# Optimization experiments

Measured on AMD Instinct MI355X. Metric: run time of the kernel, lower is better.

## Reference

```python
import jax, jax.numpy as jnp
import numpy as np

N_NODES = 50000
N_EDGES = 800000
F_IN = 24
H = 128
N_GRAPHS = 100
BN_EPS = 1e-5


def setup_inputs() -> dict:
    key = jax.random.key(0)
    ks = jax.random.split(key, 12)
    x = jax.random.normal(ks[0], (N_NODES, F_IN), dtype=jnp.float32)
    edge_index = jax.random.randint(ks[1], (2, N_EDGES), 0, N_NODES, dtype=jnp.int32)
    batch = (jnp.arange(N_NODES, dtype=jnp.int32) // (N_NODES // N_GRAPHS)).astype(jnp.int32)

    def lin(k, fan_in, fan_out):
        bound = 1.0 / np.sqrt(fan_in)
        kw, kb = jax.random.split(k)
        W = jax.random.uniform(kw, (fan_in, fan_out), jnp.float32, -bound, bound)
        b = jax.random.uniform(kb, (fan_out,), jnp.float32, -bound, bound)
        return W, b

    W1, b1 = lin(ks[2], 2 * F_IN, H)
    W2, b2 = lin(ks[3], 2 * H, H)
    W3, b3 = lin(ks[4], 2 * H, H)
    Wl, bl = lin(ks[5], H, 1)
    g1 = jnp.ones((H,), jnp.float32); be1 = jnp.zeros((H,), jnp.float32)
    g2 = jnp.ones((H,), jnp.float32); be2 = jnp.zeros((H,), jnp.float32)
    g3 = jnp.ones((H,), jnp.float32); be3 = jnp.zeros((H,), jnp.float32)
    return {"x": x, "edge_index": edge_index, "batch": batch,
            "W1": W1, "b1": b1, "W2": W2, "b2": b2, "W3": W3, "b3": b3,
            "g1": g1, "be1": be1, "g2": g2, "be2": be2, "g3": g3, "be3": be3,
            "Wl": Wl, "bl": bl}


def edge_conv(x, src, dst, W, b):
    # PyG EdgeConv: message = mlp([x_i, x_j - x_i]) for edge j->i, aggr=max at i
    x_i = x[dst]                                    # [E, F]
    e = jnp.concatenate([x_i, x[src] - x_i], axis=-1)  # [E, 2F]
    m = jax.nn.relu(e @ W + b)                      # [E, H]
    out = jax.ops.segment_max(m, dst, num_segments=N_NODES)
    return jnp.where(jnp.isfinite(out), out, 0.0)   # isolated nodes -> 0


def batch_norm(h, g, b):
    # training-mode BN over node dim (biased variance), dropout treated as identity
    mu = h.mean(axis=0)
    var = ((h - mu) ** 2).mean(axis=0)
    return g * (h - mu) * jax.lax.rsqrt(var + BN_EPS) + b


def reference(x, edge_index, batch, W1, b1, W2, b2, W3, b3,
              g1, be1, g2, be2, g3, be3, Wl, bl):
    src, dst = edge_index[0], edge_index[1]
    h = edge_conv(x, src, dst, W1, b1)
    h = jax.nn.relu(batch_norm(h, g1, be1))
    h = edge_conv(h, src, dst, W2, b2)
    h = jax.nn.relu(batch_norm(h, g2, be2))
    h = edge_conv(h, src, dst, W3, b3)
    h = batch_norm(h, g3, be3)
    # global_mean_pool
    sums = jax.ops.segment_sum(h, batch, num_segments=N_GRAPHS)           # [G, H]
    counts = jax.ops.segment_sum(jnp.ones((h.shape[0],), h.dtype), batch,
                                 num_segments=N_GRAPHS)
    pooled = sums / jnp.maximum(counts, 1.0)[:, None]
    return jax.nn.relu(pooled @ Wl + bl)                                  # [G, 1]
```

## Files before the change

kernel.cpp:

```cpp
#include <hip/hip_runtime.h>

#define N_NODES 50000
#define N_EDGES 800000
#define F_IN 24
#define HDIM 128
#define N_GRAPHS 100
#define BN_EPS 1e-5f
#define NBLK 196
#define ROWS_PER_GRAPH (N_NODES / N_GRAPHS)
#define MM_GRID 782
#define HIST_BLKS ((N_EDGES + 255) / 256)
#define PREP_BLKS (F_IN + 2 * HDIM)
#define SSTR 32
#define SUMS_PER_LAYER (256 * SSTR)
#define STATS_BLKS 196

typedef _Float16 h2 __attribute__((ext_vector_type(2)));
typedef _Float16 h4 __attribute__((ext_vector_type(4)));
typedef _Float16 f16x8 __attribute__((ext_vector_type(8)));
typedef float f32x4 __attribute__((ext_vector_type(4)));

template <int K, int KC>
__global__ __launch_bounds__(256) void k_mm1(const float* __restrict__ X,
                                             const float* __restrict__ Wcat,
                                             const float* __restrict__ bias,
                                             float* __restrict__ A, _Float16* __restrict__ C) {
    __shared__ float Xs[KC * 68];
    __shared__ float Ws[KC * 128];
    int tid = threadIdx.x;
    int row0 = blockIdx.x * 64;
    const bool isA = (blockIdx.y == 0);
    const int colbase = isA ? 0 : 128;
    int cg = tid & 31;
    int rg = tid >> 5;

    float acc[8][4];
#pragma unroll
    for (int ri = 0; ri < 8; ++ri)
#pragma unroll
        for (int ci = 0; ci < 4; ++ci)
            acc[ri][ci] = isA ? bias[cg * 4 + ci] : 0.f;

    for (int k0 = 0; k0 < K; k0 += KC) {
        __syncthreads();
        {
            const int C4 = KC / 4;
            for (int i = tid; i < 64 * C4; i += 256) {
                int c4 = i % C4, r = i / C4;
                int row = row0 + r;
                float4 v = make_float4(0.f, 0.f, 0.f, 0.f);
                if (row < N_NODES) v = *(const float4*)&X[row * K + k0 + c4 * 4];
                Xs[(c4 * 4 + 0) * 68 + r] = v.x;
                Xs[(c4 * 4 + 1) * 68 + r] = v.y;
                Xs[(c4 * 4 + 2) * 68 + r] = v.z;
                Xs[(c4 * 4 + 3) * 68 + r] = v.w;
            }
        }
        for (int i = tid; i < KC * 32; i += 256) {
            int c4 = i & 31, kr = i >> 5;
            *(float4*)&Ws[kr * 128 + c4 * 4] =
                *(const float4*)&Wcat[(k0 + kr) * 256 + colbase + c4 * 4];
        }
        __syncthreads();
#pragma unroll
        for (int kk = 0; kk < KC; ++kk) {
            float4 t0 = *(const float4*)&Xs[kk * 68 + rg * 8];
            float4 t1 = *(const float4*)&Xs[kk * 68 + rg * 8 + 4];
            float4 w = *(const float4*)&Ws[kk * 128 + cg * 4];
            float t[8] = {t0.x, t0.y, t0.z, t0.w, t1.x, t1.y, t1.z, t1.w};
            float wv[4] = {w.x, w.y, w.z, w.w};
#pragma unroll
            for (int ri = 0; ri < 8; ++ri)
#pragma unroll
                for (int ci = 0; ci < 4; ++ci)
                    acc[ri][ci] += t[ri] * wv[ci];
        }
    }

#pragma unroll
    for (int ri = 0; ri < 8; ++ri) {
        int row = row0 + rg * 8 + ri;
        if (row < N_NODES) {
            if (isA) {
                *(float4*)&A[row * HDIM + cg * 4] =
                    make_float4(acc[ri][0], acc[ri][1], acc[ri][2], acc[ri][3]);
            } else {
                union { h2 h[2]; uint2 u; } pk;
                pk.h[0] = h2{(_Float16)acc[ri][0], (_Float16)acc[ri][1]};
                pk.h[1] = h2{(_Float16)acc[ri][2], (_Float16)acc[ri][3]};
                *(uint2*)&C[row * HDIM + cg * 4] = pk.u;
            }
        }
    }
}

__global__ __launch_bounds__(256) void k_mmf(const _Float16* __restrict__ X,
                                             const _Float16* __restrict__ Wf,
                                             const float* __restrict__ bias,
                                             const float* __restrict__ sums,
                                             const float* __restrict__ g,
                                             const float* __restrict__ be,
                                             float* __restrict__ A, _Float16* __restrict__ C) {
    __shared__ _Float16 Xh[16 * 520];
    __shared__ _Float16 Wh[128 * 128];
    __shared__ float scs[128], shs[128];
    int tid = threadIdx.x;
    int lane = tid & 63, wv = tid >> 6;
    int row0 = blockIdx.x * 64;
    const bool isA = (blockIdx.y == 0);
    const _Float16* Wsrc = Wf + (isA ? 0 : 16384);

    if (tid < 128) {
        float S  = sums[tid * SSTR];
        float S2 = sums[(128 + tid) * SSTR];
        float mean = S / (float)N_NODES;
        float var = fmaxf(S2 / (float)N_NODES - mean * mean, 0.f);
        float scv = g[tid] / sqrtf(var + BN_EPS);
        scs[tid] = scv;
        shs[tid] = be[tid] - mean * scv;
    }
    {
        const uint4* s = (const uint4*)Wsrc;
        uint4* d = (uint4*)Wh;
        for (int i = tid; i < 2048; i += 256) d[i] = s[i];
    }
    __syncthreads();
    for (int i = tid; i < 64 * 32; i += 256) {
        int k4 = i & 31, rl = i >> 5;
        int row = row0 + rl;
        float4 v = make_float4(0.f, 0.f, 0.f, 0.f);
        if (row < N_NODES) {
            h4 xv = *(const h4*)&X[row * HDIM + k4 * 4];
            v = make_float4((float)xv.x, (float)xv.y, (float)xv.z, (float)xv.w);
        }
        int c = k4 * 4;
        v.x = fmaxf(v.x * scs[c + 0] + shs[c + 0], 0.f);
        v.y = fmaxf(v.y * scs[c + 1] + shs[c + 1], 0.f);
        v.z = fmaxf(v.z * scs[c + 2] + shs[c + 2], 0.f);
        v.w = fmaxf(v.w * scs[c + 3] + shs[c + 3], 0.f);
        int rt = rl >> 4, m = rl & 15, kc = k4 >> 3, q = (k4 >> 1) & 3, jh = k4 & 1;
        _Float16* d = Xh + (rt * 4 + kc) * 520 + (q * 16 + m) * 8 + jh * 4;
        d[0] = (_Float16)v.x; d[1] = (_Float16)v.y;
        d[2] = (_Float16)v.z; d[3] = (_Float16)v.w;
    }
    __syncthreads();

    int n = lane & 15, q = lane >> 4;
    f32x4 acc[8];
#pragma unroll
    for (int nt = 0; nt < 8; ++nt) {
        float b0 = isA ? bias[nt * 16 + n] : 0.f;
        acc[nt] = f32x4{b0, b0, b0, b0};
    }
#pragma unroll
    for (int kc = 0; kc < 4; ++kc) {
        f16x8 a = *(const f16x8*)(Xh + (wv * 4 + kc) * 520 + lane * 8);
#pragma unroll
        for (int nt = 0; nt < 8; ++nt) {
            f16x8 b = *(const f16x8*)(Wh + ((nt * 4 + kc) * 64 + lane) * 8);
            acc[nt] = __builtin_amdgcn_mfma_f32_16x16x32_f16(a, b, acc[nt], 0, 0, 0);
        }
    }
#pragma unroll
    for (int nt = 0; nt < 8; ++nt) {
#pragma unroll
        for (int r = 0; r < 4; ++r) {
            int row = row0 + wv * 16 + q * 4 + r;
            if (row < N_NODES) {
                int col = nt * 16 + n;
                if (isA) A[row * HDIM + col] = acc[nt][r];
                else     C[row * HDIM + col] = (_Float16)acc[nt][r];
            }
        }
    }
}

__global__ void k_pre(const float* __restrict__ W1, const float* __restrict__ W2,
                      const float* __restrict__ W3, float* __restrict__ Wcat1,
                      _Float16* __restrict__ Wf2, _Float16* __restrict__ Wf3,
                      const int* __restrict__ dst, unsigned* __restrict__ deg,
                      unsigned* __restrict__ rank) {
    int b = blockIdx.x;
    int j = threadIdx.x;
    if (b < F_IN) {
        float wb = W1[(b + F_IN) * HDIM + (j & 127)];
        float wt = W1[b * HDIM + (j & 127)];
        Wcat1[b * 256 + j] = (j < HDIM) ? (wt - wb) : wb;
    } else if (b < PREP_BLKS) {
        int idx = b - F_IN;
        int layer = idx >> 7;
        int k = idx & 127;
        const float* W = layer ? W3 : W2;
        _Float16* Wf   = layer ? Wf3 : Wf2;
        int col = j & 127;
        float wt = W[k * HDIM + col];
        float wb = W[(k + HDIM) * HDIM + col];
        float v = (j < 128) ? (wt - wb) : wb;
        int plane = j >> 7;
        int nt = col >> 4, n = col & 15, kc = k >> 5, q = (k >> 3) & 3, jj = k & 7;
        int f = ((nt * 4 + kc) * 4 + q) * 128 + n * 8 + jj;
        Wf[plane * 16384 + f] = (_Float16)v;
    } else {
        int e = (b - PREP_BLKS) * 256 + j;
        if (e < N_EDGES) rank[e] = atomicAdd(&deg[dst[e]], 1u);
    }
}

__global__ __launch_bounds__(256) void k_scanall(const unsigned* __restrict__ deg,
                                                 unsigned* __restrict__ bsum,
                                                 unsigned* __restrict__ off) {
    __shared__ unsigned s[256];
    int t = threadIdx.x;
    int b = blockIdx.x;
    int i = b * 256 + t;
    unsigned v = (i < N_NODES) ? deg[i] : 0u;
    s[t] = v;
    __syncthreads();
    for (int d = 1; d < 256; d <<= 1) {
        unsigned u = (t >= d) ? s[t - d] : 0u;
        __syncthreads();
        s[t] += u;
        __syncthreads();
    }
    unsigned locex = s[t] - v;
    if (t == 255) atomicExch(&bsum[b], s[255] + 1u);
    __syncthreads();
    unsigned bs = 0;
    if (t < NBLK) {
        unsigned x;
        do { x = atomicAdd(&bsum[t], 0u); } while (x == 0u);
        bs = x - 1u;
    }
    s[t] = (t < NBLK) ? bs : 0u;
    __syncthreads();
    for (int d = 1; d < 256; d <<= 1) {
        unsigned u = (t >= d) ? s[t - d] : 0u;
        __syncthreads();
        s[t] += u;
        __syncthreads();
    }
    unsigned bexcl = (b == 0) ? 0u : s[b - 1];
    if (i < N_NODES) off[i] = bexcl + locex;
}

__global__ void k_scatter(const int* __restrict__ src, const int* __restrict__ dst,
                          const unsigned* __restrict__ off, const unsigned* __restrict__ rank,
                          unsigned* __restrict__ ssrc) {
    int e = blockIdx.x * 256 + threadIdx.x;
    if (e < N_EDGES)
        ssrc[off[dst[e]] + rank[e]] = (unsigned)src[e];
}

__global__ __launch_bounds__(256) void k_agg(const float* __restrict__ A,
                                             const h2* __restrict__ Cc,
                                             const unsigned* __restrict__ off,
                                             const unsigned* __restrict__ deg,
                                             const unsigned* __restrict__ ssrc,
                                             h2* __restrict__ H) {
    __shared__ unsigned sl[4][64];
    int w = threadIdx.x >> 6;
    int lane = threadIdx.x & 63;
    int i = blockIdx.x * 4 + w;
    int d = (int)deg[i];
    unsigned o = off[i];
    union { unsigned short us[2]; h2 v; } ninf;
    ninf.us[0] = 0xFC00; ninf.us[1] = 0xFC00;
    h2 m2 = ninf.v;
    for (int base = 0; base < d; base += 64) {
        int cntc = min(64, d - base);
        if (lane < cntc) sl[w][lane] = ssrc[o + base + lane];
        int e = 0;
        for (; e + 8 <= cntc; e += 8) {
            unsigned s0 = sl[w][e + 0], s1 = sl[w][e + 1], s2 = sl[w][e + 2], s3 = sl[w][e + 3];
            unsigned s4 = sl[w][e + 4], s5 = sl[w][e + 5], s6 = sl[w][e + 6], s7 = sl[w][e + 7];
            h2 v0 = Cc[s0 * 64 + lane];
            h2 v1 = Cc[s1 * 64 + lane];
            h2 v2 = Cc[s2 * 64 + lane];
            h2 v3 = Cc[s3 * 64 + lane];
            h2 v4 = Cc[s4 * 64 + lane];
            h2 v5 = Cc[s5 * 64 + lane];
            h2 v6 = Cc[s6 * 64 + lane];
            h2 v7 = Cc[s7 * 64 + lane];
            h2 a0 = __builtin_elementwise_max(v0, v1);
            h2 a1 = __builtin_elementwise_max(v2, v3);
            h2 a2 = __builtin_elementwise_max(v4, v5);
            h2 a3 = __builtin_elementwise_max(v6, v7);
            h2 b0 = __builtin_elementwise_max(a0, a1);
            h2 b1 = __builtin_elementwise_max(a2, a3);
            m2 = __builtin_elementwise_max(m2, __builtin_elementwise_max(b0, b1));
        }
        if (e + 4 <= cntc) {
            unsigned s0 = sl[w][e + 0], s1 = sl[w][e + 1], s2 = sl[w][e + 2], s3 = sl[w][e + 3];
            h2 v0 = Cc[s0 * 64 + lane];
            h2 v1 = Cc[s1 * 64 + lane];
            h2 v2 = Cc[s2 * 64 + lane];
            h2 v3 = Cc[s3 * 64 + lane];
            h2 a0 = __builtin_elementwise_max(v0, v1);
            h2 a1 = __builtin_elementwise_max(v2, v3);
            m2 = __builtin_elementwise_max(m2, __builtin_elementwise_max(a0, a1));
            e += 4;
        }
        for (; e < cntc; ++e)
            m2 = __builtin_elementwise_max(m2, Cc[sl[w][e] * 64 + lane]);
    }
    float2 a = *(const float2*)&A[i * HDIM + lane * 2];
    float hx = (d > 0) ? fmaxf(a.x + (float)m2.x, 0.f) : 0.f;
    float hy = (d > 0) ? fmaxf(a.y + (float)m2.y, 0.f) : 0.f;
    H[i * 64 + lane] = h2{(_Float16)hx, (_Float16)hy};
}

__global__ __launch_bounds__(256) void k_stats(const _Float16* __restrict__ H,
                                               float* __restrict__ sums) {
    __shared__ float4 ls[256], ls2[256];
    int t = threadIdx.x;
    int c4 = t & 31, rg = t >> 5;
    int row0 = blockIdx.x * 256;
    float4 s = make_float4(0.f, 0.f, 0.f, 0.f);
    float4 s2 = make_float4(0.f, 0.f, 0.f, 0.f);
#pragma unroll 4
    for (int it = 0; it < 32; ++it) {
        int row = row0 + rg * 32 + it;
        if (row < N_NODES) {
            h4 hv = *(const h4*)&H[row * HDIM + c4 * 4];
            float4 v = make_float4((float)hv.x, (float)hv.y, (float)hv.z, (float)hv.w);
            s.x += v.x; s.y += v.y; s.z += v.z; s.w += v.w;
            s2.x += v.x * v.x; s2.y += v.y * v.y; s2.z += v.z * v.z; s2.w += v.w * v.w;
        }
    }
    ls[t] = s; ls2[t] = s2;
    __syncthreads();
    if (t < 32) {
        float4 a = ls[t], a2 = ls2[t];
#pragma unroll
        for (int j = 1; j < 8; ++j) {
            float4 b = ls[j * 32 + t], b2 = ls2[j * 32 + t];
            a.x += b.x; a.y += b.y; a.z += b.z; a.w += b.w;
            a2.x += b2.x; a2.y += b2.y; a2.z += b2.z; a2.w += b2.w;
        }
        int c = t * 4;
        atomicAdd(&sums[(c + 0) * SSTR], a.x);
        atomicAdd(&sums[(c + 1) * SSTR], a.y);
        atomicAdd(&sums[(c + 2) * SSTR], a.z);
        atomicAdd(&sums[(c + 3) * SSTR], a.w);
        atomicAdd(&sums[(128 + c + 0) * SSTR], a2.x);
        atomicAdd(&sums[(128 + c + 1) * SSTR], a2.y);
        atomicAdd(&sums[(128 + c + 2) * SSTR], a2.z);
        atomicAdd(&sums[(128 + c + 3) * SSTR], a2.w);
    }
}

__global__ __launch_bounds__(128) void k_poolsum(const _Float16* __restrict__ H,
                                                 float* __restrict__ Pg,
                                                 float* __restrict__ sums) {
    int g = blockIdx.x;
    int k = threadIdx.x;
    const _Float16* base = H + (size_t)g * ROWS_PER_GRAPH * HDIM;
    float s = 0.f, s2 = 0.f;
#pragma unroll 4
    for (int r = 0; r < ROWS_PER_GRAPH; ++r) {
        float v = (float)base[r * HDIM + k];
        s += v; s2 += v * v;
    }
    Pg[g * HDIM + k] = s;
    atomicAdd(&sums[k * SSTR], s);
    atomicAdd(&sums[(128 + k) * SSTR], s2);
}

__global__ __launch_bounds__(128) void k_out(const float* __restrict__ Pg,
                                             const float* __restrict__ sums,
                                             const float* __restrict__ g3,
                                             const float* __restrict__ be3,
                                             const float* __restrict__ Wl,
                                             const float* __restrict__ bl,
                                             float* __restrict__ out) {
    int g = blockIdx.x;
    int k = threadIdx.x;
    float S  = sums[k * SSTR];
    float S2 = sums[(128 + k) * SSTR];
    float mean = S / (float)N_NODES;
    float var = fmaxf(S2 / (float)N_NODES - mean * mean, 0.f);
    float scv = g3[k] / sqrtf(var + BN_EPS);
    float shv = be3[k] - mean * scv;
    float p = (scv * (Pg[g * HDIM + k] * (1.f / (float)ROWS_PER_GRAPH)) + shv) * Wl[k];
    __shared__ float red[2];
    for (int o = 32; o > 0; o >>= 1) p += __shfl_down(p, o);
    if ((k & 63) == 0) red[k >> 6] = p;
    __syncthreads();
    if (k == 0) out[g] = fmaxf(red[0] + red[1] + bl[0], 0.f);
}

extern "C" void kernel_launch(void* const* d_in, const int* in_sizes, int n_in,
                              void* d_out, int out_size, void* d_ws, size_t ws_size,
                              hipStream_t stream) {
    const float* x   = (const float*)d_in[0];
    const int* ei    = (const int*)d_in[1];
    const float* W1  = (const float*)d_in[3];
    const float* b1  = (const float*)d_in[4];
    const float* W2  = (const float*)d_in[5];
    const float* b2  = (const float*)d_in[6];
    const float* W3  = (const float*)d_in[7];
    const float* b3  = (const float*)d_in[8];
    const float* g1  = (const float*)d_in[9];
    const float* be1 = (const float*)d_in[10];
    const float* g2  = (const float*)d_in[11];
    const float* be2 = (const float*)d_in[12];
    const float* g3  = (const float*)d_in[13];
    const float* be3 = (const float*)d_in[14];
    const float* Wl  = (const float*)d_in[15];
    const float* bl  = (const float*)d_in[16];
    float* out = (float*)d_out;

    const int* srcp = ei;
    const int* dstp = ei + N_EDGES;

    char* ws = (char*)d_ws;
    size_t o = 0;
    auto alloc = [&](size_t bytes) -> void* {
        o = (o + 255) & ~(size_t)255;
        void* p = ws + o;
        o += bytes;
        return p;
    };
    float* A      = (float*)alloc((size_t)N_NODES * HDIM * 4);
    _Float16* C   = (_Float16*)alloc((size_t)N_NODES * HDIM * 2);
    _Float16* h   = (_Float16*)alloc((size_t)N_NODES * HDIM * 2);
    float* Wcat1  = (float*)alloc((size_t)F_IN * 256 * 4);
    _Float16* Wf2 = (_Float16*)alloc((size_t)2 * 16384 * 2);
    _Float16* Wf3 = (_Float16*)alloc((size_t)2 * 16384 * 2);
    unsigned* deg  = (unsigned*)alloc((size_t)N_NODES * 4);
    unsigned* bsum = (unsigned*)alloc((size_t)NBLK * 4);
    float* sums    = (float*)alloc((size_t)3 * SUMS_PER_LAYER * 4);
    unsigned* off  = (unsigned*)alloc((size_t)N_NODES * 4);
    unsigned* rank = (unsigned*)alloc((size_t)N_EDGES * 4);
    unsigned* ssrc = (unsigned*)alloc((size_t)N_EDGES * 4);
    float* Pg      = (float*)alloc((size_t)N_GRAPHS * HDIM * 4);
    (void)ws_size; (void)n_in; (void)in_sizes; (void)out_size;

    float* sums0 = sums;
    float* sums1 = sums + SUMS_PER_LAYER;
    float* sums2 = sums + 2 * SUMS_PER_LAYER;

    size_t zlen = (size_t)((char*)(sums + 3 * SUMS_PER_LAYER) - (char*)deg);
    (void)hipMemsetAsync(deg, 0, zlen, stream);

    k_pre<<<PREP_BLKS + HIST_BLKS, 256, 0, stream>>>(W1, W2, W3, Wcat1, Wf2, Wf3,
                                                     dstp, deg, rank);
    k_scanall<<<NBLK, 256, 0, stream>>>(deg, bsum, off);
    k_scatter<<<HIST_BLKS, 256, 0, stream>>>(srcp, dstp, off, rank, ssrc);

    const dim3 MMG(MM_GRID, 2);
    const int AGB = N_NODES / 4;

    k_mm1<F_IN, F_IN><<<MMG, 256, 0, stream>>>(x, Wcat1, b1, A, C);
    k_agg<<<AGB, 256, 0, stream>>>(A, (const h2*)C, off, deg, ssrc, (h2*)h);
    k_stats<<<STATS_BLKS, 256, 0, stream>>>(h, sums0);

    k_mmf<<<MMG, 256, 0, stream>>>(h, Wf2, b2, sums0, g1, be1, A, C);
    k_agg<<<AGB, 256, 0, stream>>>(A, (const h2*)C, off, deg, ssrc, (h2*)h);
    k_stats<<<STATS_BLKS, 256, 0, stream>>>(h, sums1);

    k_mmf<<<MMG, 256, 0, stream>>>(h, Wf3, b3, sums1, g2, be2, A, C);
    k_agg<<<AGB, 256, 0, stream>>>(A, (const h2*)C, off, deg, ssrc, (h2*)h);

    k_poolsum<<<N_GRAPHS, 128, 0, stream>>>(h, Pg, sums2);
    k_out<<<N_GRAPHS, 128, 0, stream>>>(Pg, sums2, g3, be3, Wl, bl, out);
}
```

Baseline: 400.4 us.

## Fuse BN statistics and mean-pool accumulation into aggregation kernel epilogue

Removes the separate k_stats and k_poolsum kernels and computes per-channel sum and sum-of-squares inside k_agg's epilogue. The partial sums are spread across 98 group slots per channel to cut atomic contention, and consumers (k_mmf, k_out) reduce those slots on load. The aim is to avoid re-reading h from memory and to save two kernel launches per layer. In exchange, stats now use fp32 values before fp16 rounding, each k_agg block adds a barrier plus atomics, and every mmf block re-reduces the partial slots.

```diff
diff --git a/kernel.cpp b/kernel.cpp
--- a/kernel.cpp
+++ b/kernel.cpp
@@ -11,9 +11,9 @@
 #define MM_GRID 782
 #define HIST_BLKS ((N_EDGES + 255) / 256)
 #define PREP_BLKS (F_IN + 2 * HDIM)
-#define SSTR 32
-#define SUMS_PER_LAYER (256 * SSTR)
-#define STATS_BLKS 196
+#define AGB (N_NODES / 4)
+#define NGRP 98
+#define SGRP 104
 
 typedef _Float16 h2 __attribute__((ext_vector_type(2)));
 typedef _Float16 h4 __attribute__((ext_vector_type(4)));
@@ -97,12 +97,13 @@
 __global__ __launch_bounds__(256) void k_mmf(const _Float16* __restrict__ X,
                                              const _Float16* __restrict__ Wf,
                                              const float* __restrict__ bias,
-                                             const float* __restrict__ sums,
+                                             const float* __restrict__ sumsP,
                                              const float* __restrict__ g,
                                              const float* __restrict__ be,
                                              float* __restrict__ A, _Float16* __restrict__ C) {
     __shared__ _Float16 Xh[16 * 520];
     __shared__ _Float16 Wh[128 * 128];
+    __shared__ float Srow[256];
     __shared__ float scs[128], shs[128];
     int tid = threadIdx.x;
     int lane = tid & 63, wv = tid >> 6;
@@ -110,19 +111,31 @@
     const bool isA = (blockIdx.y == 0);
     const _Float16* Wsrc = Wf + (isA ? 0 : 16384);
 
+    {
+        const float* rp = sumsP + tid * SGRP;
+        float s = 0.f;
+#pragma unroll
+        for (int j = 0; j < 24; ++j) {
+            float4 v = *(const float4*)&rp[j * 4];
+            s += v.x + v.y + v.z + v.w;
+        }
+        s += rp[96] + rp[97];
+        Srow[tid] = s;
+    }
+    {
+        const uint4* s = (const uint4*)Wsrc;
+        uint4* d = (uint4*)Wh;
+        for (int i = tid; i < 2048; i += 256) d[i] = s[i];
+    }
+    __syncthreads();
     if (tid < 128) {
-        float S  = sums[tid * SSTR];
-        float S2 = sums[(128 + tid) * SSTR];
+        float S  = Srow[tid];
+        float S2 = Srow[128 + tid];
         float mean = S / (float)N_NODES;
         float var = fmaxf(S2 / (float)N_NODES - mean * mean, 0.f);
         float scv = g[tid] / sqrtf(var + BN_EPS);
         scs[tid] = scv;
         shs[tid] = be[tid] - mean * scv;
-    }
-    {
-        const uint4* s = (const uint4*)Wsrc;
-        uint4* d = (uint4*)Wh;
-        for (int i = tid; i < 2048; i += 256) d[i] = s[i];
     }
     __syncthreads();
     for (int i = tid; i < 64 * 32; i += 256) {
@@ -251,13 +264,18 @@
         ssrc[off[dst[e]] + rank[e]] = (unsigned)src[e];
 }
 
+template <bool POOL>
 __global__ __launch_bounds__(256) void k_agg(const float* __restrict__ A,
                                              const h2* __restrict__ Cc,
                                              const unsigned* __restrict__ off,
                                              const unsigned* __restrict__ deg,
                                              const unsigned* __restrict__ ssrc,
-                                             h2* __restrict__ H) {
+                                             h2* __restrict__ H,
+                                             float* __restrict__ sumsP,
+                                             float* __restrict__ Pg) {
     __shared__ unsigned sl[4][64];
+    __shared__ float2 ps[4][64];
+    __shared__ float2 ps2[4][64];
     int w = threadIdx.x >> 6;
     int lane = threadIdx.x & 63;
     int i = blockIdx.x * 4 + w;
@@ -307,67 +325,33 @@
     float hx = (d > 0) ? fmaxf(a.x + (float)m2.x, 0.f) : 0.f;
     float hy = (d > 0) ? fmaxf(a.y + (float)m2.y, 0.f) : 0.f;
     H[i * 64 + lane] = h2{(_Float16)hx, (_Float16)hy};
-}
-
-__global__ __launch_bounds__(256) void k_stats(const _Float16* __restrict__ H,
-                                               float* __restrict__ sums) {
-    __shared__ float4 ls[256], ls2[256];
-    int t = threadIdx.x;
-    int c4 = t & 31, rg = t >> 5;
-    int row0 = blockIdx.x * 256;
-    float4 s = make_float4(0.f, 0.f, 0.f, 0.f);
-    float4 s2 = make_float4(0.f, 0.f, 0.f, 0.f);
-#pragma unroll 4
-    for (int it = 0; it < 32; ++it) {
-        int row = row0 + rg * 32 + it;
-        if (row < N_NODES) {
-            h4 hv = *(const h4*)&H[row * HDIM + c4 * 4];
-            float4 v = make_float4((float)hv.x, (float)hv.y, (float)hv.z, (float)hv.w);
-            s.x += v.x; s.y += v.y; s.z += v.z; s.w += v.w;
-            s2.x += v.x * v.x; s2.y += v.y * v.y; s2.z += v.z * v.z; s2.w += v.w * v.w;
-        }
-    }
-    ls[t] = s; ls2[t] = s2;
-    __syncthreads();
-    if (t < 32) {
-        float4 a = ls[t], a2 = ls2[t];
-#pragma unroll
-        for (int j = 1; j < 8; ++j) {
-            float4 b = ls[j * 32 + t], b2 = ls2[j * 32 + t];
-            a.x += b.x; a.y += b.y; a.z += b.z; a.w += b.w;
-            a2.x += b2.x; a2.y += b2.y; a2.z += b2.z; a2.w += b2.w;
-        }
-        int c = t * 4;
-        atomicAdd(&sums[(c + 0) * SSTR], a.x);
-        atomicAdd(&sums[(c + 1) * SSTR], a.y);
-        atomicAdd(&sums[(c + 2) * SSTR], a.z);
-        atomicAdd(&sums[(c + 3) * SSTR], a.w);
-        atomicAdd(&sums[(128 + c + 0) * SSTR], a2.x);
-        atomicAdd(&sums[(128 + c + 1) * SSTR], a2.y);
-        atomicAdd(&sums[(128 + c + 2) * SSTR], a2.z);
-        atomicAdd(&sums[(128 + c + 3) * SSTR], a2.w);
-    }
-}
-
-__global__ __launch_bounds__(128) void k_poolsum(const _Float16* __restrict__ H,
-                                                 float* __restrict__ Pg,
-                                                 float* __restrict__ sums) {
-    int g = blockIdx.x;
-    int k = threadIdx.x;
-    const _Float16* base = H + (size_t)g * ROWS_PER_GRAPH * HDIM;
-    float s = 0.f, s2 = 0.f;
-#pragma unroll 4
-    for (int r = 0; r < ROWS_PER_GRAPH; ++r) {
-        float v = (float)base[r * HDIM + k];
-        s += v; s2 += v * v;
-    }
-    Pg[g * HDIM + k] = s;
-    atomicAdd(&sums[k * SSTR], s);
-    atomicAdd(&sums[(128 + k) * SSTR], s2);
+
+    ps[w][lane]  = float2{hx, hy};
+    ps2[w][lane] = float2{hx * hx, hy * hy};
+    __syncthreads();
+    if (w == 0) {
+        float sx = 0.f, sy = 0.f, qx = 0.f, qy = 0.f;
+#pragma unroll
+        for (int j = 0; j < 4; ++j) {
+            float2 p = ps[j][lane], p2 = ps2[j][lane];
+            sx += p.x; sy += p.y; qx += p2.x; qy += p2.y;
+        }
+        int grp = blockIdx.x >> 7;
+        int c0 = lane * 2;
+        atomicAdd(&sumsP[(c0 + 0) * SGRP + grp], sx);
+        atomicAdd(&sumsP[(c0 + 1) * SGRP + grp], sy);
+        atomicAdd(&sumsP[(128 + c0) * SGRP + grp], qx);
+        atomicAdd(&sumsP[(129 + c0) * SGRP + grp], qy);
+        if (POOL) {
+            int graph = (blockIdx.x * 4) / ROWS_PER_GRAPH;
+            atomicAdd(&Pg[graph * HDIM + c0], sx);
+            atomicAdd(&Pg[graph * HDIM + c0 + 1], sy);
+        }
+    }
 }
 
 __global__ __launch_bounds__(128) void k_out(const float* __restrict__ Pg,
-                                             const float* __restrict__ sums,
+                                             const float* __restrict__ sumsP,
                                              const float* __restrict__ g3,
                                              const float* __restrict__ be3,
                                              const float* __restrict__ Wl,
@@ -375,8 +359,18 @@
                                              float* __restrict__ out) {
     int g = blockIdx.x;
     int k = threadIdx.x;
-    float S  = sums[k * SSTR];
-    float S2 = sums[(128 + k) * SSTR];
+    const float* r1 = sumsP + k * SGRP;
+    const float* r2 = sumsP + (128 + k) * SGRP;
+    float S = 0.f, S2 = 0.f;
+#pragma unroll
+    for (int j = 0; j < 24; ++j) {
+        float4 a = *(const float4*)&r1[j * 4];
+        float4 b = *(const float4*)&r2[j * 4];
+        S  += a.x + a.y + a.z + a.w;
+        S2 += b.x + b.y + b.z + b.w;
+    }
+    S  += r1[96] + r1[97];
+    S2 += r2[96] + r2[97];
     float mean = S / (float)N_NODES;
     float var = fmaxf(S2 / (float)N_NODES - mean * mean, 0.f);
     float scv = g3[k] / sqrtf(var + BN_EPS);
@@ -429,18 +423,16 @@
     _Float16* Wf3 = (_Float16*)alloc((size_t)2 * 16384 * 2);
     unsigned* deg  = (unsigned*)alloc((size_t)N_NODES * 4);
     unsigned* bsum = (unsigned*)alloc((size_t)NBLK * 4);
-    float* sums    = (float*)alloc((size_t)3 * SUMS_PER_LAYER * 4);
+    float* sums0P  = (float*)alloc((size_t)256 * SGRP * 4);
+    float* sums1P  = (float*)alloc((size_t)256 * SGRP * 4);
+    float* sums2P  = (float*)alloc((size_t)256 * SGRP * 4);
+    float* Pg      = (float*)alloc((size_t)N_GRAPHS * HDIM * 4);
     unsigned* off  = (unsigned*)alloc((size_t)N_NODES * 4);
     unsigned* rank = (unsigned*)alloc((size_t)N_EDGES * 4);
     unsigned* ssrc = (unsigned*)alloc((size_t)N_EDGES * 4);
-    float* Pg      = (float*)alloc((size_t)N_GRAPHS * HDIM * 4);
     (void)ws_size; (void)n_in; (void)in_sizes; (void)out_size;
 
-    float* sums0 = sums;
-    float* sums1 = sums + SUMS_PER_LAYER;
-    float* sums2 = sums + 2 * SUMS_PER_LAYER;
-
-    size_t zlen = (size_t)((char*)(sums + 3 * SUMS_PER_LAYER) - (char*)deg);
+    size_t zlen = (size_t)((char*)(Pg + (size_t)N_GRAPHS * HDIM) - (char*)deg);
     (void)hipMemsetAsync(deg, 0, zlen, stream);
 
     k_pre<<<PREP_BLKS + HIST_BLKS, 256, 0, stream>>>(W1, W2, W3, Wcat1, Wf2, Wf3,
@@ -449,19 +441,18 @@
     k_scatter<<<HIST_BLKS, 256, 0, stream>>>(srcp, dstp, off, rank, ssrc);
 
     const dim3 MMG(MM_GRID, 2);
-    const int AGB = N_NODES / 4;
 
     k_mm1<F_IN, F_IN><<<MMG, 256, 0, stream>>>(x, Wcat1, b1, A, C);
-    k_agg<<<AGB, 256, 0, stream>>>(A, (const h2*)C, off, deg, ssrc, (h2*)h);
-    k_stats<<<STATS_BLKS, 256, 0, stream>>>(h, sums0);
-
-    k_mmf<<<MMG, 256, 0, stream>>>(h, Wf2, b2, sums0, g1, be1, A, C);
-    k_agg<<<AGB, 256, 0, stream>>>(A, (const h2*)C, off, deg, ssrc, (h2*)h);
-    k_stats<<<STATS_BLKS, 256, 0, stream>>>(h, sums1);
-
-    k_mmf<<<MMG, 256, 0, stream>>>(h, Wf3, b3, sums1, g2, be2, A, C);
-    k_agg<<<AGB, 256, 0, stream>>>(A, (const h2*)C, off, deg, ssrc, (h2*)h);
-
-    k_poolsum<<<N_GRAPHS, 128, 0, stream>>>(h, Pg, sums2);
-    k_out<<<N_GRAPHS, 128, 0, stream>>>(Pg, sums2, g3, be3, Wl, bl, out);
-}
+    k_agg<false><<<AGB, 256, 0, stream>>>(A, (const h2*)C, off, deg, ssrc, (h2*)h,
+                                          sums0P, nullptr);
+
+    k_mmf<<<MMG, 256, 0, stream>>>(h, Wf2, b2, sums0P, g1, be1, A, C);
+    k_agg<false><<<AGB, 256, 0, stream>>>(A, (const h2*)C, off, deg, ssrc, (h2*)h,
+                                          sums1P, nullptr);
+
+    k_mmf<<<MMG, 256, 0, stream>>>(h, Wf3, b3, sums1P, g2, be2, A, C);
+    k_agg<true><<<AGB, 256, 0, stream>>>(A, (const h2*)C, off, deg, ssrc, (h2*)h,
+                                         sums2P, Pg);
+
+    k_out<<<N_GRAPHS, 128, 0, stream>>>(Pg, sums2P, g3, be3, Wl, bl, out);
+}
```

Result: slower. 1.060 ms (+164.7%).
